# Performance work log

Hardware: AMD Instinct MI355X
Metric: run time of the kernel (lower is better)

## Reference

```python
import jax, jax.numpy as jnp
import numpy as np

N = 50000      # nodes
E = 800000     # edges (before self-loops)
F_IN = 128     # num_node_features
H = 4          # heads
C = 64         # hidden_channels
G = 64         # graphs in batch
OUT = 5


def setup_inputs():
    key = jax.random.key(0)
    ks = jax.random.split(key, 16)
    s = 0.1
    def rn(k, shape, sc=s):
        return jax.random.normal(k, shape, dtype=jnp.float32) * sc
    return {
        "x": rn(ks[0], (N, F_IN), 1.0),
        "edge_index": jax.random.randint(ks[1], (2, E), 0, N, dtype=jnp.int32),
        "batch": jnp.sort(jax.random.randint(ks[2], (N,), 0, G, dtype=jnp.int32)),
        "W1": rn(ks[3], (F_IN, H * C)), "a1s": rn(ks[4], (H, C)), "a1d": rn(ks[5], (H, C)), "b1": jnp.zeros((H * C,), jnp.float32),
        "g1": jnp.ones((H * C,), jnp.float32), "be1": jnp.zeros((H * C,), jnp.float32),
        "W2": rn(ks[6], (H * C, H * C)), "a2s": rn(ks[7], (H, C)), "a2d": rn(ks[8], (H, C)), "b2": jnp.zeros((H * C,), jnp.float32),
        "g2": jnp.ones((H * C,), jnp.float32), "be2": jnp.zeros((H * C,), jnp.float32),
        "W3": rn(ks[9], (H * C, C)), "a3s": rn(ks[10], (1, C)), "a3d": rn(ks[11], (1, C)), "b3": jnp.zeros((C,), jnp.float32),
        "g3": jnp.ones((C,), jnp.float32), "be3": jnp.zeros((C,), jnp.float32),
        "Wg": rn(ks[12], (C, 128)), "bg": jnp.zeros((128,), jnp.float32),
        "Wg2": rn(ks[13], (128, 64)), "bg2": jnp.zeros((64,), jnp.float32),
        "Wo": rn(ks[14], (64, OUT)), "bo": jnp.zeros((OUT,), jnp.float32),
    }


def _layer_norm(x, g, b, eps=1e-5):
    mu = jnp.mean(x, axis=-1, keepdims=True)
    var = jnp.mean((x - mu) ** 2, axis=-1, keepdims=True)
    return (x - mu) * jax.lax.rsqrt(var + eps) * g + b


def _gat_conv(x, src, dst, W, a_s, a_d, b, heads, c, concat):
    # PyG GATConv (eval mode, dropout inactive): linear -> per-edge scores ->
    # segment softmax over incoming edges of each dst -> scatter-sum aggregation.
    n = x.shape[0]
    h = (x @ W).reshape(n, heads, c)                 # [N,H,C]
    alpha_src = jnp.sum(h * a_s, axis=-1)            # [N,H]
    alpha_dst = jnp.sum(h * a_d, axis=-1)            # [N,H]
    e = jax.nn.leaky_relu(alpha_src[src] + alpha_dst[dst], 0.2)   # [E',H]
    emax = jax.ops.segment_max(e, dst, num_segments=n)            # [N,H]
    ex = jnp.exp(e - emax[dst])
    denom = jax.ops.segment_sum(ex, dst, num_segments=n)
    alpha = ex / denom[dst]                          # softmax per dst (self-loops guarantee denom>0)
    out = jax.ops.segment_sum(alpha[:, :, None] * h[src], dst, num_segments=n)  # [N,H,C]
    out = out.reshape(n, heads * c) if concat else out.mean(axis=1)
    return out + b


def reference(x, edge_index, batch, W1, a1s, a1d, b1, g1, be1, W2, a2s, a2d, b2, g2, be2, W3, a3s, a3d, b3, g3, be3, Wg, bg, Wg2, bg2, Wo, bo):
    n = x.shape[0]
    loop = jnp.arange(n, dtype=edge_index.dtype)
    src = jnp.concatenate([edge_index[0], loop])     # GATConv adds self-loops
    dst = jnp.concatenate([edge_index[1], loop])
    h = _gat_conv(x, src, dst, W1, a1s, a1d, b1, H, C, True)
    h = jax.nn.elu(_layer_norm(h, g1, be1))
    h = _gat_conv(h, src, dst, W2, a2s, a2d, b2, H, C, True)
    h = jax.nn.elu(_layer_norm(h, g2, be2))
    h = _gat_conv(h, src, dst, W3, a3s, a3d, b3, 1, C, False)
    h = jax.nn.elu(_layer_norm(h, g3, be3))
    # global_mean_pool over graph ids
    sums = jax.ops.segment_sum(h, batch, num_segments=G)
    cnt = jax.ops.segment_sum(jnp.ones((n,), h.dtype), batch, num_segments=G)
    gm = sums / jnp.maximum(cnt, 1.0)[:, None]
    z = jax.nn.relu(gm @ Wg + bg)
    z = jax.nn.relu(z @ Wg2 + bg2)
    return z @ Wo + bo
```

## Files before the change

kernel.cpp:

```cpp
#include <hip/hip_runtime.h>
#include <math.h>

typedef _Float16 half2v __attribute__((ext_vector_type(2)));
typedef _Float16 half4v __attribute__((ext_vector_type(4)));
typedef _Float16 half8v __attribute__((ext_vector_type(8)));
typedef float floatx4 __attribute__((ext_vector_type(4)));

static __device__ __forceinline__ half2v pack_rtz(float a, float b) {
  return __builtin_bit_cast(half2v, __builtin_amdgcn_cvt_pkrtz(a, b));
}
static __device__ __forceinline__ float dot2(half2v w, unsigned hi, unsigned lo, unsigned sel, float acc) {
  return __builtin_amdgcn_fdot2(w, __builtin_bit_cast(half2v, __builtin_amdgcn_perm(hi, lo, sel)), acc, false);
}

__global__ __launch_bounds__(256) void prep_kernel(const float* __restrict__ W1,
                                                   const float* __restrict__ W2,
                                                   const float* __restrict__ W3,
                                                   const float* __restrict__ x,
                                                   _Float16* __restrict__ Wt1,
                                                   _Float16* __restrict__ Wt2,
                                                   _Float16* __restrict__ Wt3,
                                                   _Float16* __restrict__ x16, int n8) {
  int b = blockIdx.x;
  int t = threadIdx.x;
  if (b < 256) {
    if (t < 128) Wt1[(size_t)b * 128 + t] = (_Float16)W1[(size_t)t * 256 + b];
  } else if (b < 512) {
    int col = b - 256;
    Wt2[(size_t)col * 256 + t] = (_Float16)W2[(size_t)t * 256 + col];
  } else if (b < 576) {
    int col = b - 512;
    Wt3[(size_t)col * 256 + t] = (_Float16)W3[(size_t)t * 64 + col];
  } else {
    int i = (b - 576) * 256 + t;
    if (i < n8) {
      float4 a = ((const float4*)x)[2 * i];
      float4 c = ((const float4*)x)[2 * i + 1];
      half8v h = {(_Float16)a.x, (_Float16)a.y, (_Float16)a.z, (_Float16)a.w,
                  (_Float16)c.x, (_Float16)c.y, (_Float16)c.z, (_Float16)c.w};
      ((half8v*)x16)[i] = h;
    }
  }
}

__global__ void count_kernel(const int* __restrict__ ei, int E, int N, int* __restrict__ counts) {
  int e = blockIdx.x * 256 + threadIdx.x;
  if (e >= E + N) return;
  int d = (e < E) ? ei[E + e] : (e - E);
  atomicAdd(&counts[d], 1);
}

__global__ __launch_bounds__(1024) void scan1_kernel(const int* __restrict__ counts,
                                                     int* __restrict__ offsets,
                                                     int* __restrict__ blocksums, int n) {
  __shared__ int wsum[16];
  int tid = threadIdx.x, lane = tid & 63, wid = tid >> 6;
  int i = blockIdx.x * 1024 + tid;
  int v = (i < n) ? counts[i] : 0;
  int x = v;
  #pragma unroll
  for (int off = 1; off < 64; off <<= 1) {
    int t = __shfl_up(x, off);
    if (lane >= off) x += t;
  }
  if (lane == 63) wsum[wid] = x;
  __syncthreads();
  if (wid == 0) {
    int w = (lane < 16) ? wsum[lane] : 0;
    #pragma unroll
    for (int off = 1; off < 16; off <<= 1) {
      int t = __shfl_up(w, off);
      if (lane >= off) w += t;
    }
    if (lane < 16) wsum[lane] = w;
  }
  __syncthreads();
  int wpre = (wid > 0) ? wsum[wid - 1] : 0;
  if (i < n) offsets[i] = wpre + x - v;
  if (tid == 0) blocksums[blockIdx.x] = wsum[15];
}

__global__ __launch_bounds__(1024) void scan2_kernel(int* __restrict__ blocksums,
                                                     int* __restrict__ offsets, int nb, int n) {
  __shared__ int wsum[16];
  int tid = threadIdx.x, lane = tid & 63, wid = tid >> 6;
  int v = (tid < nb) ? blocksums[tid] : 0;
  int x = v;
  #pragma unroll
  for (int off = 1; off < 64; off <<= 1) {
    int t = __shfl_up(x, off);
    if (lane >= off) x += t;
  }
  if (lane == 63) wsum[wid] = x;
  __syncthreads();
  if (wid == 0) {
    int w = (lane < 16) ? wsum[lane] : 0;
    #pragma unroll
    for (int off = 1; off < 16; off <<= 1) {
      int t = __shfl_up(w, off);
      if (lane >= off) w += t;
    }
    if (lane < 16) wsum[lane] = w;
  }
  __syncthreads();
  int wpre = (wid > 0) ? wsum[wid - 1] : 0;
  if (tid < nb) blocksums[tid] = wpre + x - v;
  if (tid == 0) offsets[n] = wsum[15];
}

__global__ void scan3_kernel(int* __restrict__ offsets, int* __restrict__ cursor,
                             const int* __restrict__ blocksums, int n) {
  int i = blockIdx.x * 256 + threadIdx.x;
  if (i < n) {
    int o = offsets[i] + blocksums[i >> 10];
    offsets[i] = o;
    cursor[i] = o;
  }
}

__global__ void scatter_kernel(const int* __restrict__ ei, int E, int N,
                               int* __restrict__ cursor, int* __restrict__ src_csr) {
  int e = blockIdx.x * 256 + threadIdx.x;
  if (e >= E + N) return;
  int s = (e < E) ? ei[e] : (e - E);
  int d = (e < E) ? ei[E + e] : (e - E);
  int pos = atomicAdd(&cursor[d], 1);
  src_csr[pos] = s;
}

template <int NT, int H>
__global__ __launch_bounds__(256) void gemm16_kernel(const _Float16* __restrict__ A,
                                                     const _Float16* __restrict__ Wt,
                                                     const float* __restrict__ als,
                                                     const float* __restrict__ ald,
                                                     _Float16* __restrict__ out16,
                                                     float* __restrict__ asrc,
                                                     float* __restrict__ adst,
                                                     int M, int K) {
  constexpr int Nc = NT * 16;
  constexpr int BM = 128, BK = 32;
  constexpr int CPH = NT / H;
  __shared__ _Float16 As[BM][40];
  __shared__ _Float16 Ws[Nc][40];
  int bm = blockIdx.x * BM;
  int tid = threadIdx.x;
  int w = tid >> 6, l = tid & 63;
  int lr = l & 15, lg = l >> 4;

  floatx4 acc[2][NT];
  #pragma unroll
  for (int rf = 0; rf < 2; ++rf)
    #pragma unroll
    for (int ct = 0; ct < NT; ++ct) acc[rf][ct] = (floatx4){0.f, 0.f, 0.f, 0.f};

  for (int k0 = 0; k0 < K; k0 += BK) {
    #pragma unroll
    for (int i = 0; i < 2; ++i) {
      int idx = tid + i * 256;
      int r = idx >> 2, c8 = idx & 3;
      int gr = bm + r;
      half8v hv = {(_Float16)0, (_Float16)0, (_Float16)0, (_Float16)0,
                   (_Float16)0, (_Float16)0, (_Float16)0, (_Float16)0};
      if (gr < M) hv = *(const half8v*)&A[(size_t)gr * K + k0 + c8 * 8];
      *(half8v*)&As[r][c8 * 8] = hv;
    }
    #pragma unroll
    for (int i = 0; i < NT / 4; ++i) {
      int idx = tid + i * 256;
      int col = idx >> 2, c8 = idx & 3;
      *(half8v*)&Ws[col][c8 * 8] = *(const half8v*)&Wt[(size_t)col * K + k0 + c8 * 8];
    }
    __syncthreads();
    half8v a0 = *(half8v*)&As[w * 32 + lr][lg * 8];
    half8v a1 = *(half8v*)&As[w * 32 + 16 + lr][lg * 8];
    #pragma unroll
    for (int ct = 0; ct < NT; ++ct) {
      half8v b = *(half8v*)&Ws[ct * 16 + lr][lg * 8];
      acc[0][ct] = __builtin_amdgcn_mfma_f32_16x16x32_f16(a0, b, acc[0][ct], 0, 0, 0);
      acc[1][ct] = __builtin_amdgcn_mfma_f32_16x16x32_f16(a1, b, acc[1][ct], 0, 0, 0);
    }
    __syncthreads();
  }
  float als_r[NT], ald_r[NT];
  #pragma unroll
  for (int ct = 0; ct < NT; ++ct) {
    als_r[ct] = als[ct * 16 + lr];
    ald_r[ct] = ald[ct * 16 + lr];
  }
  #pragma unroll
  for (int rf = 0; rf < 2; ++rf)
    #pragma unroll
    for (int q = 0; q < 4; ++q) {
      int row = bm + w * 32 + rf * 16 + lg * 4 + q;
      float ps[H], pd[H];
      #pragma unroll
      for (int hh = 0; hh < H; ++hh) {
        float s = 0.f, d = 0.f;
        #pragma unroll
        for (int c2 = 0; c2 < CPH; ++c2) {
          int ct = hh * CPH + c2;
          s += acc[rf][ct][q] * als_r[ct];
          d += acc[rf][ct][q] * ald_r[ct];
        }
        ps[hh] = s; pd[hh] = d;
      }
      #pragma unroll
      for (int off = 1; off < 16; off <<= 1) {
        #pragma unroll
        for (int hh = 0; hh < H; ++hh) {
          ps[hh] += __shfl_xor(ps[hh], off);
          pd[hh] += __shfl_xor(pd[hh], off);
        }
      }
      if (row < M) {
        if (lr == 0) {
          #pragma unroll
          for (int hh = 0; hh < H; ++hh) asrc[row * H + hh] = ps[hh];
        } else if (lr == 1) {
          #pragma unroll
          for (int hh = 0; hh < H; ++hh) adst[row * H + hh] = pd[hh];
        }
        #pragma unroll
        for (int ct = 0; ct < NT; ++ct)
          out16[(size_t)row * Nc + ct * 16 + lr] = (_Float16)acc[rf][ct][q];
      }
    }
}

__global__ __launch_bounds__(128) void agg4_ln_kernel(const _Float16* __restrict__ h16,
                                                      const float* __restrict__ asrc,
                                                      const float* __restrict__ adst,
                                                      const int* __restrict__ offsets,
                                                      const int* __restrict__ src_csr,
                                                      const float* __restrict__ bias,
                                                      const float* __restrict__ g,
                                                      const float* __restrict__ be,
                                                      _Float16* __restrict__ out, int n) {
  int wid = threadIdx.x >> 6, lane = threadIdx.x & 63;
  int node = blockIdx.x * 2 + wid;
  if (node >= n) return;
  int start = offsets[node], end = offsets[node + 1];
  int hl = lane >> 5;
  int l5 = lane & 31;
  int head = l5 >> 3;
  float adh = adst[node * 4 + head];
  const uint4* h4 = (const uint4*)h16;
  const half2v ones = {(_Float16)1.f, (_Float16)1.f};
  float acc[8] = {0.f, 0.f, 0.f, 0.f, 0.f, 0.f, 0.f, 0.f};
  float denom = 0.f;
  int i = start + hl;
  for (; i + 6 < end; i += 8) {
    int s0 = src_csr[i], s1 = src_csr[i + 2], s2 = src_csr[i + 4], s3 = src_csr[i + 6];
    uint4 x0 = h4[(size_t)s0 * 32 + l5];
    uint4 x1 = h4[(size_t)s1 * 32 + l5];
    uint4 x2 = h4[(size_t)s2 * 32 + l5];
    uint4 x3 = h4[(size_t)s3 * 32 + l5];
    float sc0 = asrc[s0 * 4 + head] + adh;
    float sc1 = asrc[s1 * 4 + head] + adh;
    float sc2 = asrc[s2 * 4 + head] + adh;
    float sc3 = asrc[s3 * 4 + head] + adh;
    sc0 = (sc0 >= 0.f) ? sc0 : 0.2f * sc0;
    sc1 = (sc1 >= 0.f) ? sc1 : 0.2f * sc1;
    sc2 = (sc2 >= 0.f) ? sc2 : 0.2f * sc2;
    sc3 = (sc3 >= 0.f) ? sc3 : 0.2f * sc3;
    half2v wa = pack_rtz(__expf(sc0), __expf(sc1));
    half2v wb = pack_rtz(__expf(sc2), __expf(sc3));
    denom = __builtin_amdgcn_fdot2(wa, ones, denom, false);
    denom = __builtin_amdgcn_fdot2(wb, ones, denom, false);
    acc[0] = dot2(wa, x1.x, x0.x, 0x05040100u, acc[0]);
    acc[1] = dot2(wa, x1.x, x0.x, 0x07060302u, acc[1]);
    acc[2] = dot2(wa, x1.y, x0.y, 0x05040100u, acc[2]);
    acc[3] = dot2(wa, x1.y, x0.y, 0x07060302u, acc[3]);
    acc[4] = dot2(wa, x1.z, x0.z, 0x05040100u, acc[4]);
    acc[5] = dot2(wa, x1.z, x0.z, 0x07060302u, acc[5]);
    acc[6] = dot2(wa, x1.w, x0.w, 0x05040100u, acc[6]);
    acc[7] = dot2(wa, x1.w, x0.w, 0x07060302u, acc[7]);
    acc[0] = dot2(wb, x3.x, x2.x, 0x05040100u, acc[0]);
    acc[1] = dot2(wb, x3.x, x2.x, 0x07060302u, acc[1]);
    acc[2] = dot2(wb, x3.y, x2.y, 0x05040100u, acc[2]);
    acc[3] = dot2(wb, x3.y, x2.y, 0x07060302u, acc[3]);
    acc[4] = dot2(wb, x3.z, x2.z, 0x05040100u, acc[4]);
    acc[5] = dot2(wb, x3.z, x2.z, 0x07060302u, acc[5]);
    acc[6] = dot2(wb, x3.w, x2.w, 0x05040100u, acc[6]);
    acc[7] = dot2(wb, x3.w, x2.w, 0x07060302u, acc[7]);
  }
  for (; i + 2 < end; i += 4) {
    int s0 = src_csr[i], s1 = src_csr[i + 2];
    uint4 x0 = h4[(size_t)s0 * 32 + l5];
    uint4 x1 = h4[(size_t)s1 * 32 + l5];
    float sc0 = asrc[s0 * 4 + head] + adh;
    float sc1 = asrc[s1 * 4 + head] + adh;
    sc0 = (sc0 >= 0.f) ? sc0 : 0.2f * sc0;
    sc1 = (sc1 >= 0.f) ? sc1 : 0.2f * sc1;
    half2v wa = pack_rtz(__expf(sc0), __expf(sc1));
    denom = __builtin_amdgcn_fdot2(wa, ones, denom, false);
    acc[0] = dot2(wa, x1.x, x0.x, 0x05040100u, acc[0]);
    acc[1] = dot2(wa, x1.x, x0.x, 0x07060302u, acc[1]);
    acc[2] = dot2(wa, x1.y, x0.y, 0x05040100u, acc[2]);
    acc[3] = dot2(wa, x1.y, x0.y, 0x07060302u, acc[3]);
    acc[4] = dot2(wa, x1.z, x0.z, 0x05040100u, acc[4]);
    acc[5] = dot2(wa, x1.z, x0.z, 0x07060302u, acc[5]);
    acc[6] = dot2(wa, x1.w, x0.w, 0x05040100u, acc[6]);
    acc[7] = dot2(wa, x1.w, x0.w, 0x07060302u, acc[7]);
  }
  if (i < end) {
    int s0 = src_csr[i];
    uint4 x0 = h4[(size_t)s0 * 32 + l5];
    float sc0 = asrc[s0 * 4 + head] + adh;
    sc0 = (sc0 >= 0.f) ? sc0 : 0.2f * sc0;
    half2v wa = pack_rtz(__expf(sc0), 0.f);
    denom = __builtin_amdgcn_fdot2(wa, ones, denom, false);
    acc[0] = dot2(wa, x0.x, x0.x, 0x05040100u, acc[0]);
    acc[1] = dot2(wa, x0.x, x0.x, 0x07060302u, acc[1]);
    acc[2] = dot2(wa, x0.y, x0.y, 0x05040100u, acc[2]);
    acc[3] = dot2(wa, x0.y, x0.y, 0x07060302u, acc[3]);
    acc[4] = dot2(wa, x0.z, x0.z, 0x05040100u, acc[4]);
    acc[5] = dot2(wa, x0.z, x0.z, 0x07060302u, acc[5]);
    acc[6] = dot2(wa, x0.w, x0.w, 0x05040100u, acc[6]);
    acc[7] = dot2(wa, x0.w, x0.w, 0x07060302u, acc[7]);
  }
  #pragma unroll
  for (int j = 0; j < 8; ++j) acc[j] += __shfl_xor(acc[j], 32);
  denom += __shfl_xor(denom, 32);
  float inv = 1.f / denom;
  float o[8];
  float4 b0 = *(const float4*)&bias[l5 * 8];
  float4 b1 = *(const float4*)&bias[l5 * 8 + 4];
  o[0] = acc[0] * inv + b0.x; o[1] = acc[1] * inv + b0.y;
  o[2] = acc[2] * inv + b0.z; o[3] = acc[3] * inv + b0.w;
  o[4] = acc[4] * inv + b1.x; o[5] = acc[5] * inv + b1.y;
  o[6] = acc[6] * inv + b1.z; o[7] = acc[7] * inv + b1.w;
  float s = 0.f;
  #pragma unroll
  for (int j = 0; j < 8; ++j) s += o[j];
  #pragma unroll
  for (int off = 16; off; off >>= 1) s += __shfl_xor(s, off);
  float mu = s * (1.f / 256.f);
  float var = 0.f;
  #pragma unroll
  for (int j = 0; j < 8; ++j) { float d = o[j] - mu; var += d * d; }
  #pragma unroll
  for (int off = 16; off; off >>= 1) var += __shfl_xor(var, off);
  float r = rsqrtf(var * (1.f / 256.f) + 1e-5f);
  float4 g0 = *(const float4*)&g[l5 * 8];
  float4 g1 = *(const float4*)&g[l5 * 8 + 4];
  float4 e0 = *(const float4*)&be[l5 * 8];
  float4 e1 = *(const float4*)&be[l5 * 8 + 4];
  float gg[8] = {g0.x, g0.y, g0.z, g0.w, g1.x, g1.y, g1.z, g1.w};
  float ee[8] = {e0.x, e0.y, e0.z, e0.w, e1.x, e1.y, e1.z, e1.w};
  if (hl == 0) {
    half8v yv;
    #pragma unroll
    for (int j = 0; j < 8; ++j) {
      float t = (o[j] - mu) * r * gg[j] + ee[j];
      t = (t > 0.f) ? t : expm1f(t);
      yv[j] = (_Float16)t;
    }
    *(half8v*)&out[(size_t)node * 256 + l5 * 8] = yv;
  }
}

__global__ __launch_bounds__(128) void agg1_ln_kernel(const _Float16* __restrict__ h16,
                                                      const float* __restrict__ asrc,
                                                      const float* __restrict__ adst,
                                                      const int* __restrict__ offsets,
                                                      const int* __restrict__ src_csr,
                                                      const float* __restrict__ bias,
                                                      const float* __restrict__ g,
                                                      const float* __restrict__ be,
                                                      float* __restrict__ out, int n) {
  int wid = threadIdx.x >> 6, lane = threadIdx.x & 63;
  int node = blockIdx.x * 2 + wid;
  if (node >= n) return;
  int start = offsets[node], end = offsets[node + 1];
  int qi = lane >> 4;
  int ql = lane & 15;
  float adh = adst[node];
  const uint2* h2 = (const uint2*)h16;
  const half2v ones = {(_Float16)1.f, (_Float16)1.f};
  float acc[4] = {0.f, 0.f, 0.f, 0.f};
  float denom = 0.f;
  int i = start + qi;
  for (; i + 12 < end; i += 16) {
    int s0 = src_csr[i], s1 = src_csr[i + 4], s2 = src_csr[i + 8], s3 = src_csr[i + 12];
    uint2 x0 = h2[(size_t)s0 * 16 + ql];
    uint2 x1 = h2[(size_t)s1 * 16 + ql];
    uint2 x2 = h2[(size_t)s2 * 16 + ql];
    uint2 x3 = h2[(size_t)s3 * 16 + ql];
    float sc0 = asrc[s0] + adh;
    float sc1 = asrc[s1] + adh;
    float sc2 = asrc[s2] + adh;
    float sc3 = asrc[s3] + adh;
    sc0 = (sc0 >= 0.f) ? sc0 : 0.2f * sc0;
    sc1 = (sc1 >= 0.f) ? sc1 : 0.2f * sc1;
    sc2 = (sc2 >= 0.f) ? sc2 : 0.2f * sc2;
    sc3 = (sc3 >= 0.f) ? sc3 : 0.2f * sc3;
    half2v wa = pack_rtz(__expf(sc0), __expf(sc1));
    half2v wb = pack_rtz(__expf(sc2), __expf(sc3));
    denom = __builtin_amdgcn_fdot2(wa, ones, denom, false);
    denom = __builtin_amdgcn_fdot2(wb, ones, denom, false);
    acc[0] = dot2(wa, x1.x, x0.x, 0x05040100u, acc[0]);
    acc[1] = dot2(wa, x1.x, x0.x, 0x07060302u, acc[1]);
    acc[2] = dot2(wa, x1.y, x0.y, 0x05040100u, acc[2]);
    acc[3] = dot2(wa, x1.y, x0.y, 0x07060302u, acc[3]);
    acc[0] = dot2(wb, x3.x, x2.x, 0x05040100u, acc[0]);
    acc[1] = dot2(wb, x3.x, x2.x, 0x07060302u, acc[1]);
    acc[2] = dot2(wb, x3.y, x2.y, 0x05040100u, acc[2]);
    acc[3] = dot2(wb, x3.y, x2.y, 0x07060302u, acc[3]);
  }
  for (; i + 4 < end; i += 8) {
    int s0 = src_csr[i], s1 = src_csr[i + 4];
    uint2 x0 = h2[(size_t)s0 * 16 + ql];
    uint2 x1 = h2[(size_t)s1 * 16 + ql];
    float sc0 = asrc[s0] + adh;
    float sc1 = asrc[s1] + adh;
    sc0 = (sc0 >= 0.f) ? sc0 : 0.2f * sc0;
    sc1 = (sc1 >= 0.f) ? sc1 : 0.2f * sc1;
    half2v wa = pack_rtz(__expf(sc0), __expf(sc1));
    denom = __builtin_amdgcn_fdot2(wa, ones, denom, false);
    acc[0] = dot2(wa, x1.x, x0.x, 0x05040100u, acc[0]);
    acc[1] = dot2(wa, x1.x, x0.x, 0x07060302u, acc[1]);
    acc[2] = dot2(wa, x1.y, x0.y, 0x05040100u, acc[2]);
    acc[3] = dot2(wa, x1.y, x0.y, 0x07060302u, acc[3]);
  }
  if (i < end) {
    int s0 = src_csr[i];
    uint2 x0 = h2[(size_t)s0 * 16 + ql];
    float sc0 = asrc[s0] + adh;
    sc0 = (sc0 >= 0.f) ? sc0 : 0.2f * sc0;
    half2v wa = pack_rtz(__expf(sc0), 0.f);
    denom = __builtin_amdgcn_fdot2(wa, ones, denom, false);
    acc[0] = dot2(wa, x0.x, x0.x, 0x05040100u, acc[0]);
    acc[1] = dot2(wa, x0.x, x0.x, 0x07060302u, acc[1]);
    acc[2] = dot2(wa, x0.y, x0.y, 0x05040100u, acc[2]);
    acc[3] = dot2(wa, x0.y, x0.y, 0x07060302u, acc[3]);
  }
  #pragma unroll
  for (int off = 32; off >= 16; off >>= 1) {
    #pragma unroll
    for (int j = 0; j < 4; ++j) acc[j] += __shfl_xor(acc[j], off);
    denom += __shfl_xor(denom, off);
  }
  float inv = 1.f / denom;
  float4 b4 = *(const float4*)&bias[ql * 4];
  float o[4];
  o[0] = acc[0] * inv + b4.x; o[1] = acc[1] * inv + b4.y;
  o[2] = acc[2] * inv + b4.z; o[3] = acc[3] * inv + b4.w;
  float s = o[0] + o[1] + o[2] + o[3];
  #pragma unroll
  for (int off = 8; off; off >>= 1) s += __shfl_xor(s, off);
  float mu = s * (1.f / 64.f);
  float var = 0.f;
  #pragma unroll
  for (int j = 0; j < 4; ++j) { float d = o[j] - mu; var += d * d; }
  #pragma unroll
  for (int off = 8; off; off >>= 1) var += __shfl_xor(var, off);
  float r = rsqrtf(var * (1.f / 64.f) + 1e-5f);
  float4 g4 = *(const float4*)&g[ql * 4];
  float4 e4 = *(const float4*)&be[ql * 4];
  float gg[4] = {g4.x, g4.y, g4.z, g4.w};
  float ee[4] = {e4.x, e4.y, e4.z, e4.w};
  float y[4];
  #pragma unroll
  for (int j = 0; j < 4; ++j) {
    float t = (o[j] - mu) * r * gg[j] + ee[j];
    y[j] = (t > 0.f) ? t : expm1f(t);
  }
  if (qi == 0) {
    *(float4*)&out[(size_t)node * 64 + ql * 4] = make_float4(y[0], y[1], y[2], y[3]);
  }
}

__global__ __launch_bounds__(256) void graph_head_kernel(const float* __restrict__ h,
                                                         const int* __restrict__ batch, int N,
                                                         const float* __restrict__ Wg,
                                                         const float* __restrict__ bg,
                                                         const float* __restrict__ Wg2,
                                                         const float* __restrict__ bg2,
                                                         const float* __restrict__ Wo,
                                                         const float* __restrict__ bo,
                                                         float* __restrict__ out) {
  __shared__ int bounds[2];
  __shared__ float part[4][64];
  __shared__ float gm[64];
  __shared__ float z1[128];
  __shared__ float z2[64];
  int g = blockIdx.x;
  int tid = threadIdx.x;
  if (tid < 2) {
    int target = g + tid;
    int lo = 0, hi = N;
    while (lo < hi) {
      int mid = (lo + hi) >> 1;
      if (batch[mid] < target) lo = mid + 1; else hi = mid;
    }
    bounds[tid] = lo;
  }
  __syncthreads();
  int lo = bounds[0], hi = bounds[1];
  int c = tid & 63, sub = tid >> 6;
  float acc = 0.f;
  for (int r = lo + sub; r < hi; r += 4) acc += h[(size_t)r * 64 + c];
  part[sub][c] = acc;
  __syncthreads();
  float invc = 1.f / fmaxf((float)(hi - lo), 1.f);
  if (tid < 64) gm[tid] = (part[0][tid] + part[1][tid] + part[2][tid] + part[3][tid]) * invc;
  __syncthreads();
  if (tid < 128) {
    float a = bg[tid];
    for (int k = 0; k < 64; ++k) a += gm[k] * Wg[k * 128 + tid];
    z1[tid] = fmaxf(a, 0.f);
  }
  __syncthreads();
  if (tid < 64) {
    float a = bg2[tid];
    for (int k = 0; k < 128; ++k) a += z1[k] * Wg2[k * 64 + tid];
    z2[tid] = fmaxf(a, 0.f);
  }
  __syncthreads();
  if (tid < 5) {
    float a = bo[tid];
    for (int k = 0; k < 64; ++k) a += z2[k] * Wo[k * 5 + tid];
    out[g * 5 + tid] = a;
  }
}

extern "C" void kernel_launch(void* const* d_in, const int* in_sizes, int n_in,
                              void* d_out, int out_size, void* d_ws, size_t ws_size,
                              hipStream_t stream) {
  const float* x   = (const float*)d_in[0];
  const int* ei    = (const int*)d_in[1];
  const int* batch = (const int*)d_in[2];
  const float* W1  = (const float*)d_in[3];
  const float* a1s = (const float*)d_in[4];
  const float* a1d = (const float*)d_in[5];
  const float* b1  = (const float*)d_in[6];
  const float* g1  = (const float*)d_in[7];
  const float* be1 = (const float*)d_in[8];
  const float* W2  = (const float*)d_in[9];
  const float* a2s = (const float*)d_in[10];
  const float* a2d = (const float*)d_in[11];
  const float* b2  = (const float*)d_in[12];
  const float* g2  = (const float*)d_in[13];
  const float* be2 = (const float*)d_in[14];
  const float* W3  = (const float*)d_in[15];
  const float* a3s = (const float*)d_in[16];
  const float* a3d = (const float*)d_in[17];
  const float* b3  = (const float*)d_in[18];
  const float* g3  = (const float*)d_in[19];
  const float* be3 = (const float*)d_in[20];
  const float* Wg  = (const float*)d_in[21];
  const float* bg  = (const float*)d_in[22];
  const float* Wg2 = (const float*)d_in[23];
  const float* bg2 = (const float*)d_in[24];
  const float* Wo  = (const float*)d_in[25];
  const float* bo  = (const float*)d_in[26];

  const int N = in_sizes[2];
  const int E = in_sizes[1] / 2;
  const int ET = E + N;
  const int G = 64;
  const int NB = (N + 1023) / 1024;

  char* ws = (char*)d_ws;
  size_t off = 0;
  auto carve = [&](size_t bytes) {
    void* p = ws + off;
    off = (off + bytes + 255) & ~(size_t)255;
    return p;
  };
  int* counts    = (int*)carve((size_t)N * 4);
  int* offsets   = (int*)carve((size_t)(N + 1) * 4);
  int* cursor    = (int*)carve((size_t)N * 4);
  int* blocksums = (int*)carve((size_t)NB * 4);
  int* src_csr   = (int*)carve((size_t)ET * 4);
  float* asrc    = (float*)carve((size_t)N * 4 * 4);
  float* adst    = (float*)carve((size_t)N * 4 * 4);
  _Float16* x16  = (_Float16*)carve((size_t)N * 128 * 2);
  _Float16* a16  = (_Float16*)carve((size_t)N * 256 * 2);
  _Float16* h16  = (_Float16*)carve((size_t)N * 256 * 2);
  float* buf3    = (float*)carve((size_t)N * 64 * 4);
  _Float16* Wt1  = (_Float16*)carve((size_t)128 * 256 * 2);
  _Float16* Wt2  = (_Float16*)carve((size_t)256 * 256 * 2);
  _Float16* Wt3  = (_Float16*)carve((size_t)256 * 64 * 2);
  (void)ws_size;

  const int egrid = (ET + 255) / 256;
  const int ngrid2 = (N + 1) / 2;
  const int mblocks = (N + 127) / 128;
  const int ncvt = (N * 16 + 255) / 256;

  prep_kernel<<<576 + ncvt, 256, 0, stream>>>(W1, W2, W3, x, Wt1, Wt2, Wt3, x16, N * 16);

  hipMemsetAsync(counts, 0, (size_t)N * 4, stream);
  count_kernel<<<egrid, 256, 0, stream>>>(ei, E, N, counts);
  scan1_kernel<<<NB, 1024, 0, stream>>>(counts, offsets, blocksums, N);
  scan2_kernel<<<1, 1024, 0, stream>>>(blocksums, offsets, NB, N);
  scan3_kernel<<<(N + 255) / 256, 256, 0, stream>>>(offsets, cursor, blocksums, N);
  scatter_kernel<<<egrid, 256, 0, stream>>>(ei, E, N, cursor, src_csr);

  gemm16_kernel<16, 4><<<mblocks, 256, 0, stream>>>(x16, Wt1, a1s, a1d, h16, asrc, adst, N, 128);
  agg4_ln_kernel<<<ngrid2, 128, 0, stream>>>(h16, asrc, adst, offsets, src_csr, b1, g1, be1, a16, N);

  gemm16_kernel<16, 4><<<mblocks, 256, 0, stream>>>(a16, Wt2, a2s, a2d, h16, asrc, adst, N, 256);
  agg4_ln_kernel<<<ngrid2, 128, 0, stream>>>(h16, asrc, adst, offsets, src_csr, b2, g2, be2, a16, N);

  gemm16_kernel<4, 1><<<mblocks, 256, 0, stream>>>(a16, Wt3, a3s, a3d, h16, asrc, adst, N, 256);
  agg1_ln_kernel<<<ngrid2, 128, 0, stream>>>(h16, asrc, adst, offsets, src_csr, b3, g3, be3, buf3, N);

  graph_head_kernel<<<G, 256, 0, stream>>>(buf3, batch, N, Wg, bg, Wg2, bg2, Wo, bo,
                                           (float*)d_out);
}
```

Before: 399.9 us.

## Fuse edge counting into prep, transpose GEMM epilogue, widen graph pooling

The edge-count atomics are merged into the prep kernel as extra blocks, which removes one launch. The GEMM swaps MFMA operand roles so each lane holds four consecutive output columns of one node. This lets the attention dot products use float4 weights, the reduction needs only two cross-lane shuffles, and outputs are written as half4 vectors. Graph mean pooling moves to 1024-thread blocks with float4 loads and a tree reduction in shared memory, and leaky-relu becomes fmaxf. The main risk is the launch bound change on the head kernel and the correctness of the transposed accumulator layout.

```diff
diff --git a/kernel.cpp b/kernel.cpp
--- a/kernel.cpp
+++ b/kernel.cpp
@@ -20,7 +20,9 @@
                                                    _Float16* __restrict__ Wt1,
                                                    _Float16* __restrict__ Wt2,
                                                    _Float16* __restrict__ Wt3,
-                                                   _Float16* __restrict__ x16, int n8) {
+                                                   _Float16* __restrict__ x16, int n8,
+                                                   const int* __restrict__ ei, int E, int N,
+                                                   int* __restrict__ counts, int ncvt) {
   int b = blockIdx.x;
   int t = threadIdx.x;
   if (b < 256) {
@@ -31,7 +33,7 @@
   } else if (b < 576) {
     int col = b - 512;
     Wt3[(size_t)col * 256 + t] = (_Float16)W3[(size_t)t * 64 + col];
-  } else {
+  } else if (b < 576 + ncvt) {
     int i = (b - 576) * 256 + t;
     if (i < n8) {
       float4 a = ((const float4*)x)[2 * i];
@@ -40,14 +42,13 @@
                   (_Float16)c.x, (_Float16)c.y, (_Float16)c.z, (_Float16)c.w};
       ((half8v*)x16)[i] = h;
     }
-  }
-}
-
-__global__ void count_kernel(const int* __restrict__ ei, int E, int N, int* __restrict__ counts) {
-  int e = blockIdx.x * 256 + threadIdx.x;
-  if (e >= E + N) return;
-  int d = (e < E) ? ei[E + e] : (e - E);
-  atomicAdd(&counts[d], 1);
+  } else {
+    int e = (b - 576 - ncvt) * 256 + t;
+    if (e < E + N) {
+      int d = (e < E) ? ei[E + e] : (e - E);
+      atomicAdd(&counts[d], 1);
+    }
+  }
 }
 
 __global__ __launch_bounds__(1024) void scan1_kernel(const int* __restrict__ counts,
@@ -149,9 +150,9 @@
 
   floatx4 acc[2][NT];
   #pragma unroll
-  for (int rf = 0; rf < 2; ++rf)
-    #pragma unroll
-    for (int ct = 0; ct < NT; ++ct) acc[rf][ct] = (floatx4){0.f, 0.f, 0.f, 0.f};
+  for (int nf = 0; nf < 2; ++nf)
+    #pragma unroll
+    for (int ct = 0; ct < NT; ++ct) acc[nf][ct] = (floatx4){0.f, 0.f, 0.f, 0.f};
 
   for (int k0 = 0; k0 < K; k0 += BK) {
     #pragma unroll
@@ -171,60 +172,60 @@
       *(half8v*)&Ws[col][c8 * 8] = *(const half8v*)&Wt[(size_t)col * K + k0 + c8 * 8];
     }
     __syncthreads();
-    half8v a0 = *(half8v*)&As[w * 32 + lr][lg * 8];
-    half8v a1 = *(half8v*)&As[w * 32 + 16 + lr][lg * 8];
+    half8v b0 = *(half8v*)&As[w * 32 + lr][lg * 8];
+    half8v b1 = *(half8v*)&As[w * 32 + 16 + lr][lg * 8];
     #pragma unroll
     for (int ct = 0; ct < NT; ++ct) {
-      half8v b = *(half8v*)&Ws[ct * 16 + lr][lg * 8];
-      acc[0][ct] = __builtin_amdgcn_mfma_f32_16x16x32_f16(a0, b, acc[0][ct], 0, 0, 0);
-      acc[1][ct] = __builtin_amdgcn_mfma_f32_16x16x32_f16(a1, b, acc[1][ct], 0, 0, 0);
+      half8v a = *(half8v*)&Ws[ct * 16 + lr][lg * 8];
+      acc[0][ct] = __builtin_amdgcn_mfma_f32_16x16x32_f16(a, b0, acc[0][ct], 0, 0, 0);
+      acc[1][ct] = __builtin_amdgcn_mfma_f32_16x16x32_f16(a, b1, acc[1][ct], 0, 0, 0);
     }
     __syncthreads();
   }
-  float als_r[NT], ald_r[NT];
+  float4 als4[NT], ald4[NT];
   #pragma unroll
   for (int ct = 0; ct < NT; ++ct) {
-    als_r[ct] = als[ct * 16 + lr];
-    ald_r[ct] = ald[ct * 16 + lr];
-  }
-  #pragma unroll
-  for (int rf = 0; rf < 2; ++rf)
-    #pragma unroll
-    for (int q = 0; q < 4; ++q) {
-      int row = bm + w * 32 + rf * 16 + lg * 4 + q;
-      float ps[H], pd[H];
+    als4[ct] = *(const float4*)&als[ct * 16 + lg * 4];
+    ald4[ct] = *(const float4*)&ald[ct * 16 + lg * 4];
+  }
+  #pragma unroll
+  for (int nf = 0; nf < 2; ++nf) {
+    int node = bm + w * 32 + nf * 16 + lr;
+    float ps[H], pd[H];
+    #pragma unroll
+    for (int hh = 0; hh < H; ++hh) {
+      float s = 0.f, d = 0.f;
       #pragma unroll
-      for (int hh = 0; hh < H; ++hh) {
-        float s = 0.f, d = 0.f;
+      for (int c2 = 0; c2 < CPH; ++c2) {
+        int ct = hh * CPH + c2;
+        s += acc[nf][ct][0] * als4[ct].x + acc[nf][ct][1] * als4[ct].y +
+             acc[nf][ct][2] * als4[ct].z + acc[nf][ct][3] * als4[ct].w;
+        d += acc[nf][ct][0] * ald4[ct].x + acc[nf][ct][1] * ald4[ct].y +
+             acc[nf][ct][2] * ald4[ct].z + acc[nf][ct][3] * ald4[ct].w;
+      }
+      ps[hh] = s; pd[hh] = d;
+    }
+    #pragma unroll
+    for (int hh = 0; hh < H; ++hh) {
+      ps[hh] += __shfl_xor(ps[hh], 16); ps[hh] += __shfl_xor(ps[hh], 32);
+      pd[hh] += __shfl_xor(pd[hh], 16); pd[hh] += __shfl_xor(pd[hh], 32);
+    }
+    if (node < M) {
+      if (lg == 0) {
         #pragma unroll
-        for (int c2 = 0; c2 < CPH; ++c2) {
-          int ct = hh * CPH + c2;
-          s += acc[rf][ct][q] * als_r[ct];
-          d += acc[rf][ct][q] * ald_r[ct];
-        }
-        ps[hh] = s; pd[hh] = d;
+        for (int hh = 0; hh < H; ++hh) asrc[node * H + hh] = ps[hh];
+      } else if (lg == 1) {
+        #pragma unroll
+        for (int hh = 0; hh < H; ++hh) adst[node * H + hh] = pd[hh];
       }
       #pragma unroll
-      for (int off = 1; off < 16; off <<= 1) {
-        #pragma unroll
-        for (int hh = 0; hh < H; ++hh) {
-          ps[hh] += __shfl_xor(ps[hh], off);
-          pd[hh] += __shfl_xor(pd[hh], off);
-        }
+      for (int ct = 0; ct < NT; ++ct) {
+        half4v hv = {(_Float16)acc[nf][ct][0], (_Float16)acc[nf][ct][1],
+                     (_Float16)acc[nf][ct][2], (_Float16)acc[nf][ct][3]};
+        *(half4v*)&out16[(size_t)node * Nc + ct * 16 + lg * 4] = hv;
       }
-      if (row < M) {
-        if (lr == 0) {
-          #pragma unroll
-          for (int hh = 0; hh < H; ++hh) asrc[row * H + hh] = ps[hh];
-        } else if (lr == 1) {
-          #pragma unroll
-          for (int hh = 0; hh < H; ++hh) adst[row * H + hh] = pd[hh];
-        }
-        #pragma unroll
-        for (int ct = 0; ct < NT; ++ct)
-          out16[(size_t)row * Nc + ct * 16 + lr] = (_Float16)acc[rf][ct][q];
-      }
-    }
+    }
+  }
 }
 
 __global__ __launch_bounds__(128) void agg4_ln_kernel(const _Float16* __restrict__ h16,
@@ -259,10 +260,10 @@
     float sc1 = asrc[s1 * 4 + head] + adh;
     float sc2 = asrc[s2 * 4 + head] + adh;
     float sc3 = asrc[s3 * 4 + head] + adh;
-    sc0 = (sc0 >= 0.f) ? sc0 : 0.2f * sc0;
-    sc1 = (sc1 >= 0.f) ? sc1 : 0.2f * sc1;
-    sc2 = (sc2 >= 0.f) ? sc2 : 0.2f * sc2;
-    sc3 = (sc3 >= 0.f) ? sc3 : 0.2f * sc3;
+    sc0 = fmaxf(sc0, 0.2f * sc0);
+    sc1 = fmaxf(sc1, 0.2f * sc1);
+    sc2 = fmaxf(sc2, 0.2f * sc2);
+    sc3 = fmaxf(sc3, 0.2f * sc3);
     half2v wa = pack_rtz(__expf(sc0), __expf(sc1));
     half2v wb = pack_rtz(__expf(sc2), __expf(sc3));
     denom = __builtin_amdgcn_fdot2(wa, ones, denom, false);
@@ -290,8 +291,8 @@
     uint4 x1 = h4[(size_t)s1 * 32 + l5];
     float sc0 = asrc[s0 * 4 + head] + adh;
     float sc1 = asrc[s1 * 4 + head] + adh;
-    sc0 = (sc0 >= 0.f) ? sc0 : 0.2f * sc0;
-    sc1 = (sc1 >= 0.f) ? sc1 : 0.2f * sc1;
+    sc0 = fmaxf(sc0, 0.2f * sc0);
+    sc1 = fmaxf(sc1, 0.2f * sc1);
     half2v wa = pack_rtz(__expf(sc0), __expf(sc1));
     denom = __builtin_amdgcn_fdot2(wa, ones, denom, false);
     acc[0] = dot2(wa, x1.x, x0.x, 0x05040100u, acc[0]);
@@ -307,7 +308,7 @@
     int s0 = src_csr[i];
     uint4 x0 = h4[(size_t)s0 * 32 + l5];
     float sc0 = asrc[s0 * 4 + head] + adh;
-    sc0 = (sc0 >= 0.f) ? sc0 : 0.2f * sc0;
+    sc0 = fmaxf(sc0, 0.2f * sc0);
     half2v wa = pack_rtz(__expf(sc0), 0.f);
     denom = __builtin_amdgcn_fdot2(wa, ones, denom, false);
     acc[0] = dot2(wa, x0.x, x0.x, 0x05040100u, acc[0]);
@@ -391,10 +392,10 @@
     float sc1 = asrc[s1] + adh;
     float sc2 = asrc[s2] + adh;
     float sc3 = asrc[s3] + adh;
-    sc0 = (sc0 >= 0.f) ? sc0 : 0.2f * sc0;
-    sc1 = (sc1 >= 0.f) ? sc1 : 0.2f * sc1;
-    sc2 = (sc2 >= 0.f) ? sc2 : 0.2f * sc2;
-    sc3 = (sc3 >= 0.f) ? sc3 : 0.2f * sc3;
+    sc0 = fmaxf(sc0, 0.2f * sc0);
+    sc1 = fmaxf(sc1, 0.2f * sc1);
+    sc2 = fmaxf(sc2, 0.2f * sc2);
+    sc3 = fmaxf(sc3, 0.2f * sc3);
     half2v wa = pack_rtz(__expf(sc0), __expf(sc1));
     half2v wb = pack_rtz(__expf(sc2), __expf(sc3));
     denom = __builtin_amdgcn_fdot2(wa, ones, denom, false);
@@ -414,8 +415,8 @@
     uint2 x1 = h2[(size_t)s1 * 16 + ql];
     float sc0 = asrc[s0] + adh;
     float sc1 = asrc[s1] + adh;
-    sc0 = (sc0 >= 0.f) ? sc0 : 0.2f * sc0;
-    sc1 = (sc1 >= 0.f) ? sc1 : 0.2f * sc1;
+    sc0 = fmaxf(sc0, 0.2f * sc0);
+    sc1 = fmaxf(sc1, 0.2f * sc1);
     half2v wa = pack_rtz(__expf(sc0), __expf(sc1));
     denom = __builtin_amdgcn_fdot2(wa, ones, denom, false);
     acc[0] = dot2(wa, x1.x, x0.x, 0x05040100u, acc[0]);
@@ -427,7 +428,7 @@
     int s0 = src_csr[i];
     uint2 x0 = h2[(size_t)s0 * 16 + ql];
     float sc0 = asrc[s0] + adh;
-    sc0 = (sc0 >= 0.f) ? sc0 : 0.2f * sc0;
+    sc0 = fmaxf(sc0, 0.2f * sc0);
     half2v wa = pack_rtz(__expf(sc0), 0.f);
     denom = __builtin_amdgcn_fdot2(wa, ones, denom, false);
     acc[0] = dot2(wa, x0.x, x0.x, 0x05040100u, acc[0]);
@@ -471,17 +472,17 @@
   }
 }
 
-__global__ __launch_bounds__(256) void graph_head_kernel(const float* __restrict__ h,
-                                                         const int* __restrict__ batch, int N,
-                                                         const float* __restrict__ Wg,
-                                                         const float* __restrict__ bg,
-                                                         const float* __restrict__ Wg2,
-                                                         const float* __restrict__ bg2,
-                                                         const float* __restrict__ Wo,
-                                                         const float* __restrict__ bo,
-                                                         float* __restrict__ out) {
+__global__ __launch_bounds__(1024) void graph_head_kernel(const float* __restrict__ h,
+                                                          const int* __restrict__ batch, int N,
+                                                          const float* __restrict__ Wg,
+                                                          const float* __restrict__ bg,
+                                                          const float* __restrict__ Wg2,
+                                                          const float* __restrict__ bg2,
+                                                          const float* __restrict__ Wo,
+                                                          const float* __restrict__ bo,
+                                                          float* __restrict__ out) {
   __shared__ int bounds[2];
-  __shared__ float part[4][64];
+  __shared__ float part[64][16][4];
   __shared__ float gm[64];
   __shared__ float z1[128];
   __shared__ float z2[64];
@@ -498,13 +499,28 @@
   }
   __syncthreads();
   int lo = bounds[0], hi = bounds[1];
-  int c = tid & 63, sub = tid >> 6;
-  float acc = 0.f;
-  for (int r = lo + sub; r < hi; r += 4) acc += h[(size_t)r * 64 + c];
-  part[sub][c] = acc;
-  __syncthreads();
-  float invc = 1.f / fmaxf((float)(hi - lo), 1.f);
-  if (tid < 64) gm[tid] = (part[0][tid] + part[1][tid] + part[2][tid] + part[3][tid]) * invc;
+  int sub = tid >> 4, cq = tid & 15;
+  float4 acc = make_float4(0.f, 0.f, 0.f, 0.f);
+  for (int r = lo + sub; r < hi; r += 64) {
+    float4 v = *(const float4*)&h[(size_t)r * 64 + cq * 4];
+    acc.x += v.x; acc.y += v.y; acc.z += v.z; acc.w += v.w;
+  }
+  part[sub][cq][0] = acc.x; part[sub][cq][1] = acc.y;
+  part[sub][cq][2] = acc.z; part[sub][cq][3] = acc.w;
+  __syncthreads();
+  #pragma unroll
+  for (int st = 32; st >= 1; st >>= 1) {
+    if (sub < st) {
+      #pragma unroll
+      for (int j = 0; j < 4; ++j) part[sub][cq][j] += part[sub + st][cq][j];
+    }
+    __syncthreads();
+  }
+  if (tid < 16) {
+    float invc = 1.f / fmaxf((float)(hi - lo), 1.f);
+    #pragma unroll
+    for (int j = 0; j < 4; ++j) gm[tid * 4 + j] = part[0][tid][j] * invc;
+  }
   __syncthreads();
   if (tid < 128) {
     float a = bg[tid];
@@ -590,10 +606,10 @@
   const int mblocks = (N + 127) / 128;
   const int ncvt = (N * 16 + 255) / 256;
 
-  prep_kernel<<<576 + ncvt, 256, 0, stream>>>(W1, W2, W3, x, Wt1, Wt2, Wt3, x16, N * 16);
-
   hipMemsetAsync(counts, 0, (size_t)N * 4, stream);
-  count_kernel<<<egrid, 256, 0, stream>>>(ei, E, N, counts);
+  prep_kernel<<<576 + ncvt + egrid, 256, 0, stream>>>(W1, W2, W3, x, Wt1, Wt2, Wt3,
+                                                      x16, N * 16, ei, E, N, counts, ncvt);
+
   scan1_kernel<<<NB, 1024, 0, stream>>>(counts, offsets, blocksums, N);
   scan2_kernel<<<1, 1024, 0, stream>>>(blocksums, offsets, NB, N);
   scan3_kernel<<<(N + 255) / 256, 256, 0, stream>>>(offsets, cursor, blocksums, N);
@@ -608,6 +624,6 @@
   gemm16_kernel<4, 1><<<mblocks, 256, 0, stream>>>(a16, Wt3, a3s, a3d, h16, asrc, adst, N, 256);
   agg1_ln_kernel<<<ngrid2, 128, 0, stream>>>(h16, asrc, adst, offsets, src_csr, b3, g3, be3, buf3, N);
 
-  graph_head_kernel<<<G, 256, 0, stream>>>(buf3, batch, N, Wg, bg, Wg2, bg2, Wo, bo,
-                                           (float*)d_out);
-}
+  graph_head_kernel<<<G, 1024, 0, stream>>>(buf3, batch, N, Wg, bg, Wg2, bg2, Wo, bo,
+                                            (float*)d_out);
+}
```

Measured after the change: 353.3 us, median of 2. -11.7%, faster.
